# Kernel tuning notes

Measured on AMD Instinct MI355X. Metric: run time of the kernel, lower is better.

The kernel has to match this reference:

```python
import jax, jax.numpy as jnp
import numpy as np


def setup_inputs() -> dict:
    key = jax.random.key(0)
    ks = jax.random.split(key, 5)
    B, T, I, H = 32, 2048, 512, 512
    scale = 1.0 / np.sqrt(H)
    return {
        "x": jax.random.normal(ks[0], (B, T, I), dtype=jnp.float32),
        "h_0": jnp.zeros((B, H), dtype=jnp.float32),
        "Wx": jax.random.normal(ks[1], (H, I), dtype=jnp.float32) * scale,
        "bx": jax.random.normal(ks[2], (H,), dtype=jnp.float32) * scale,
        "Wh": jax.random.normal(ks[3], (H, H), dtype=jnp.float32) * scale,
        "bh": jax.random.normal(ks[4], (H,), dtype=jnp.float32) * scale,
    }


def reference(x, h_0, Wx, bx, Wh, bh):
    # Precompute input projection for all timesteps in one big GEMM: [B,T,H]
    x_proj = jnp.einsum("bti,hi->bth", x, Wx) + bx + bh

    def step(h, xp_t):  # h: [B,H], xp_t: [B,H]
        h_new = jnp.tanh(xp_t + h @ Wh.T)
        return h_new, h_new

    # scan over time axis: move T to leading dim
    h_last, outs = jax.lax.scan(step, h_0, jnp.swapaxes(x_proj, 0, 1))
    outputs = jnp.swapaxes(outs, 0, 1)  # [B,T,H]
    return outputs, h_last
```

## Files before the change

kernel.cpp:

```cpp
#include <hip/hip_runtime.h>


constexpr int Bb = 32, Tt = 2048, Ii = 512, Hh = 512;
constexpr int NP = 8;
constexpr int RP = Hh / NP;

static __device__ __forceinline__ float fast_tanh(float x) {
    float ax = fabsf(x);
    float e = __expf(-2.0f * ax);
    float r = (1.0f - e) / (1.0f + e);
    return copysignf(r, x);
}

__global__ __launch_bounds__(256, 2)
void xproj_gemm(const float* __restrict__ x, const float* __restrict__ Wx,
                const float* __restrict__ bx, const float* __restrict__ bh,
                float* __restrict__ xp)
{
    constexpr int BM = 128, BK = 16, LDT = BM + 4;
    __shared__ float As[BK][LDT];
    __shared__ float Bs[BK][LDT];

    const int tid = threadIdx.x;
    const int m0 = blockIdx.x * BM;
    const int n0 = blockIdx.y * BM;
    const int lrow = tid >> 1;
    const int lkh  = (tid & 1) * 8;
    const int tx = tid & 15, ty = tid >> 4;

    float acc[2][2][4][4] = {};

    for (int k0 = 0; k0 < Ii; k0 += BK) {
        float4 a0 = *reinterpret_cast<const float4*>(&x[(size_t)(m0 + lrow) * Ii + k0 + lkh]);
        float4 a1 = *reinterpret_cast<const float4*>(&x[(size_t)(m0 + lrow) * Ii + k0 + lkh + 4]);
        float4 b0 = *reinterpret_cast<const float4*>(&Wx[(size_t)(n0 + lrow) * Ii + k0 + lkh]);
        float4 b1 = *reinterpret_cast<const float4*>(&Wx[(size_t)(n0 + lrow) * Ii + k0 + lkh + 4]);
        __syncthreads();
        As[lkh + 0][lrow] = a0.x; As[lkh + 1][lrow] = a0.y;
        As[lkh + 2][lrow] = a0.z; As[lkh + 3][lrow] = a0.w;
        As[lkh + 4][lrow] = a1.x; As[lkh + 5][lrow] = a1.y;
        As[lkh + 6][lrow] = a1.z; As[lkh + 7][lrow] = a1.w;
        Bs[lkh + 0][lrow] = b0.x; Bs[lkh + 1][lrow] = b0.y;
        Bs[lkh + 2][lrow] = b0.z; Bs[lkh + 3][lrow] = b0.w;
        Bs[lkh + 4][lrow] = b1.x; Bs[lkh + 5][lrow] = b1.y;
        Bs[lkh + 6][lrow] = b1.z; Bs[lkh + 7][lrow] = b1.w;
        __syncthreads();
        #pragma unroll
        for (int k = 0; k < BK; ++k) {
            float4 av[2], bv[2];
            av[0] = *reinterpret_cast<const float4*>(&As[k][ty * 4]);
            av[1] = *reinterpret_cast<const float4*>(&As[k][64 + ty * 4]);
            bv[0] = *reinterpret_cast<const float4*>(&Bs[k][tx * 4]);
            bv[1] = *reinterpret_cast<const float4*>(&Bs[k][64 + tx * 4]);
            #pragma unroll
            for (int rh = 0; rh < 2; ++rh) {
                const float* ap = reinterpret_cast<const float*>(&av[rh]);
                #pragma unroll
                for (int ch = 0; ch < 2; ++ch) {
                    const float* bp = reinterpret_cast<const float*>(&bv[ch]);
                    #pragma unroll
                    for (int i = 0; i < 4; ++i)
                        #pragma unroll
                        for (int j = 0; j < 4; ++j)
                            acc[rh][ch][i][j] += ap[i] * bp[j];
                }
            }
        }
    }

    float4 bias[2];
    #pragma unroll
    for (int ch = 0; ch < 2; ++ch) {
        int cb = n0 + ch * 64 + tx * 4;
        bias[ch] = make_float4(bx[cb] + bh[cb], bx[cb + 1] + bh[cb + 1],
                               bx[cb + 2] + bh[cb + 2], bx[cb + 3] + bh[cb + 3]);
    }
    #pragma unroll
    for (int rh = 0; rh < 2; ++rh)
        #pragma unroll
        for (int i = 0; i < 4; ++i) {
            size_t row = (size_t)(m0 + rh * 64 + ty * 4 + i);
            #pragma unroll
            for (int ch = 0; ch < 2; ++ch) {
                const float* bp = reinterpret_cast<const float*>(&bias[ch]);
                float4 v = make_float4(acc[rh][ch][i][0] + bp[0], acc[rh][ch][i][1] + bp[1],
                                       acc[rh][ch][i][2] + bp[2], acc[rh][ch][i][3] + bp[3]);
                *reinterpret_cast<float4*>(&xp[row * Hh + n0 + ch * 64 + tx * 4]) = v;
            }
        }
}

__global__ void zero_xbuf(unsigned long long* __restrict__ xb)
{
    xb[(size_t)blockIdx.x * 512 + threadIdx.x] = 0ull;
}

__global__ __launch_bounds__(512, 1)
void rnn_scan_mb(const float* __restrict__ Wh, const float* __restrict__ h0,
                 float* __restrict__ out, unsigned long long* __restrict__ xbuf)
{
    const int bid = blockIdx.x;
    const int c = bid & 31;
    const int P = bid >> 5;
    const int tid = threadIdx.x;
    const int w = tid >> 6;
    const int lane = tid & 63;

    __shared__ float hscratch[NP][68];
    __shared__ float pacc[2][NP][68];

    float4 wreg[16];
    #pragma unroll
    for (int k = 0; k < 16; ++k) {
        const float* ap = &Wh[(size_t)(P * RP + lane) * Hh + w * 64 + 4 * k];
        asm volatile("global_load_dwordx4 %0, %1, off"
                     : "=v"(wreg[k]) : "v"(ap));
    }
    asm volatile("s_waitcnt vmcnt(0)" ::: "memory");

    float* ob = out + (size_t)c * Tt * Hh;
    unsigned long long* xb = xbuf + (size_t)c * 2 * Hh;

    float hcur = h0[(size_t)c * Hh + w * 64 + lane];
    float xp_cur = (w == P) ? ob[P * RP + lane] : 0.f;

    for (int t = 0; t < Tt; ++t) {
        const int d = t & 1;

        hscratch[w][lane] = hcur;
        asm volatile("s_waitcnt lgkmcnt(0)" ::: "memory");

        float a0 = 0.f, a1 = 0.f, a2 = 0.f, a3 = 0.f;
        #pragma unroll
        for (int k = 0; k < 16; k += 4) {
            float4 h0v = *reinterpret_cast<const float4*>(&hscratch[w][4 * k]);
            float4 h1v = *reinterpret_cast<const float4*>(&hscratch[w][4 * k + 4]);
            float4 h2v = *reinterpret_cast<const float4*>(&hscratch[w][4 * k + 8]);
            float4 h3v = *reinterpret_cast<const float4*>(&hscratch[w][4 * k + 12]);
            const float* w0 = reinterpret_cast<const float*>(&wreg[k]);
            const float* w1 = reinterpret_cast<const float*>(&wreg[k + 1]);
            const float* w2 = reinterpret_cast<const float*>(&wreg[k + 2]);
            const float* w3 = reinterpret_cast<const float*>(&wreg[k + 3]);
            a0 += w0[0] * h0v.x; a0 += w0[1] * h0v.y; a0 += w0[2] * h0v.z; a0 += w0[3] * h0v.w;
            a1 += w1[0] * h1v.x; a1 += w1[1] * h1v.y; a1 += w1[2] * h1v.z; a1 += w1[3] * h1v.w;
            a2 += w2[0] * h2v.x; a2 += w2[1] * h2v.y; a2 += w2[2] * h2v.z; a2 += w2[3] * h2v.w;
            a3 += w3[0] * h3v.x; a3 += w3[1] * h3v.y; a3 += w3[2] * h3v.z; a3 += w3[3] * h3v.w;
        }
        pacc[d][w][lane] = (a0 + a1) + (a2 + a3);
        __syncthreads();

        if (w == P) {
            float s = xp_cur;
            #pragma unroll
            for (int g = 0; g < NP; ++g) s += pacc[d][g][lane];
            float hval = fast_tanh(s);
            hcur = hval;
            if (t + 1 < Tt) {
                unsigned long long msg =
                    ((unsigned long long)(unsigned)(t + 1) << 32) |
                    (unsigned long long)__float_as_uint(hval);
                __hip_atomic_store(&xb[(size_t)d * Hh + P * RP + lane], msg,
                                   __ATOMIC_RELAXED, __HIP_MEMORY_SCOPE_AGENT);
                ob[(size_t)t * Hh + P * RP + lane] = hval;
                xp_cur = ob[(size_t)(t + 1) * Hh + P * RP + lane];
            } else {
                ob[(size_t)t * Hh + P * RP + lane] = hval;
                out[(size_t)Bb * Tt * Hh + (size_t)c * Hh + P * RP + lane] = hval;
            }
        } else if (t + 1 < Tt) {
            const unsigned want = (unsigned)(t + 1);
            unsigned long long msg;
            do {
                msg = __hip_atomic_load(&xb[(size_t)d * Hh + w * RP + lane],
                                        __ATOMIC_RELAXED, __HIP_MEMORY_SCOPE_AGENT);
            } while ((unsigned)(msg >> 32) != want);
            hcur = __uint_as_float((unsigned)msg);
        }
    }
}

__global__ __launch_bounds__(512)
void rnn_scan_sb(const float* __restrict__ W, const float* __restrict__ h0,
                 float* __restrict__ out)
{
    const int b = blockIdx.x;
    const int j = threadIdx.x;
    __shared__ float hsb[2][Hh];
    hsb[0][j] = h0[(size_t)b * Hh + j];
    __syncthreads();

    float* ob = out + (size_t)b * Tt * Hh;
    const float* wbase = W + (size_t)j * Hh;

    float xp_cur = ob[j];
    int cur = 0;
    for (int t = 0; t < Tt; ++t) {
        float xp_next = (t + 1 < Tt) ? ob[(size_t)(t + 1) * Hh + j] : 0.0f;
        float4 a = make_float4(xp_cur, 0.0f, 0.0f, 0.0f);
        const float* h = hsb[cur];
        #pragma unroll 8
        for (int c4 = 0; c4 < Hh / 4; ++c4) {
            float4 wv = *reinterpret_cast<const float4*>(&wbase[c4 * 4]);
            float4 hv = *reinterpret_cast<const float4*>(&h[c4 * 4]);
            a.x += wv.x * hv.x; a.y += wv.y * hv.y;
            a.z += wv.z * hv.z; a.w += wv.w * hv.w;
        }
        float hn = tanhf((a.x + a.y) + (a.z + a.w));
        hsb[cur ^ 1][j] = hn;
        ob[(size_t)t * Hh + j] = hn;
        xp_cur = xp_next;
        cur ^= 1;
        __syncthreads();
    }
    out[(size_t)Bb * Tt * Hh + (size_t)b * Hh + j] = hsb[cur][j];
}

extern "C" void kernel_launch(void* const* d_in, const int* in_sizes, int n_in,
                              void* d_out, int out_size, void* d_ws, size_t ws_size,
                              hipStream_t stream)
{
    const float* x  = (const float*)d_in[0];
    const float* h0 = (const float*)d_in[1];
    const float* Wx = (const float*)d_in[2];
    const float* bx = (const float*)d_in[3];
    const float* Wh = (const float*)d_in[4];
    const float* bh = (const float*)d_in[5];
    float* out = (float*)d_out;

    dim3 g1(Bb * Tt / 128, Hh / 128);
    xproj_gemm<<<g1, 256, 0, stream>>>(x, Wx, bx, bh, out);

    const size_t xb_bytes = (size_t)Bb * 2 * Hh * sizeof(unsigned long long);
    if (ws_size >= xb_bytes) {
        unsigned long long* xbuf = (unsigned long long*)d_ws;
        zero_xbuf<<<64, 512, 0, stream>>>(xbuf);
        void* args[] = {(void*)&Wh, (void*)&h0, (void*)&out, (void*)&xbuf};
        hipLaunchCooperativeKernel((void*)rnn_scan_mb, dim3(NP * Bb), dim3(512),
                                   args, 0, stream);
    } else {
        rnn_scan_sb<<<Bb, Hh, 0, stream>>>(Wh, h0, out);
    }
}
```

Baseline: 3.298 ms.

## Add XCD-local L2 fast path for cross-block hidden-state exchange

Each block reads its XCC id from a hardware register and publishes it. After a grid sync, each batch group checks whether all eight of its blocks sit on the same XCD. Producers now write every message twice: a plain store to an L2-local buffer and an agent-scope atomic store to a second buffer. When a group is co-located, consumers first poll the L2-local copy with sc0 loads, up to a fixed number of tries, and fall back to the device-coherent buffer otherwise. The aim is to cut the latency of the per-timestep exchange, at the cost of a duplicated store per step, a grid sync at startup, and a gain that depends on where blocks are placed.

```diff
diff --git a/kernel.cpp b/kernel.cpp
--- a/kernel.cpp
+++ b/kernel.cpp
@@ -1,4 +1,5 @@
 #include <hip/hip_runtime.h>
+#include <hip/hip_cooperative_groups.h>
 
 
 constexpr int Bb = 32, Tt = 2048, Ii = 512, Hh = 512;
@@ -97,7 +98,9 @@
 
 __global__ __launch_bounds__(512, 1)
 void rnn_scan_mb(const float* __restrict__ Wh, const float* __restrict__ h0,
-                 float* __restrict__ out, unsigned long long* __restrict__ xbuf)
+                 float* __restrict__ out, unsigned long long* __restrict__ xbL2,
+                 unsigned long long* __restrict__ xbIC,
+                 unsigned int* __restrict__ xcc_arr)
 {
     const int bid = blockIdx.x;
     const int c = bid & 31;
@@ -108,6 +111,13 @@
 
     __shared__ float hscratch[NP][68];
     __shared__ float pacc[2][NP][68];
+    __shared__ unsigned int same_sh;
+
+    unsigned int myxcc;
+    asm volatile("s_getreg_b32 %0, hwreg(20, 0, 32)" : "=s"(myxcc));
+    if (tid == 0)
+        __hip_atomic_store(&xcc_arr[bid], myxcc, __ATOMIC_RELAXED,
+                           __HIP_MEMORY_SCOPE_AGENT);
 
     float4 wreg[16];
     #pragma unroll
@@ -119,10 +129,22 @@
     asm volatile("s_waitcnt vmcnt(0)" ::: "memory");
 
     float* ob = out + (size_t)c * Tt * Hh;
-    unsigned long long* xb = xbuf + (size_t)c * 2 * Hh;
+    unsigned long long* xL = xbL2 + (size_t)c * 2 * Hh;
+    unsigned long long* xI = xbIC + (size_t)c * 2 * Hh;
 
     float hcur = h0[(size_t)c * Hh + w * 64 + lane];
     float xp_cur = (w == P) ? ob[P * RP + lane] : 0.f;
+
+    cooperative_groups::this_grid().sync();
+    if (tid == 0) {
+        unsigned int s = 1;
+        for (int p = 0; p < NP; ++p)
+            s &= (__hip_atomic_load(&xcc_arr[(p << 5) | c], __ATOMIC_RELAXED,
+                                    __HIP_MEMORY_SCOPE_AGENT) == myxcc) ? 1u : 0u;
+        same_sh = s;
+    }
+    __syncthreads();
+    const bool samexcd = (same_sh != 0);
 
     for (int t = 0; t < Tt; ++t) {
         const int d = t & 1;
@@ -159,7 +181,10 @@
                 unsigned long long msg =
                     ((unsigned long long)(unsigned)(t + 1) << 32) |
                     (unsigned long long)__float_as_uint(hval);
-                __hip_atomic_store(&xb[(size_t)d * Hh + P * RP + lane], msg,
+                unsigned long long* paL = &xL[(size_t)d * Hh + P * RP + lane];
+                asm volatile("global_store_dwordx2 %0, %1, off"
+                             :: "v"(paL), "v"(msg) : "memory");
+                __hip_atomic_store(&xI[(size_t)d * Hh + P * RP + lane], msg,
                                    __ATOMIC_RELAXED, __HIP_MEMORY_SCOPE_AGENT);
                 ob[(size_t)t * Hh + P * RP + lane] = hval;
                 xp_cur = ob[(size_t)(t + 1) * Hh + P * RP + lane];
@@ -169,12 +194,29 @@
             }
         } else if (t + 1 < Tt) {
             const unsigned want = (unsigned)(t + 1);
-            unsigned long long msg;
-            do {
-                msg = __hip_atomic_load(&xb[(size_t)d * Hh + w * RP + lane],
-                                        __ATOMIC_RELAXED, __HIP_MEMORY_SCOPE_AGENT);
-            } while ((unsigned)(msg >> 32) != want);
-            hcur = __uint_as_float((unsigned)msg);
+            bool got = false;
+            unsigned val = 0;
+            if (samexcd) {
+                const unsigned long long* paL = &xL[(size_t)d * Hh + w * RP + lane];
+                uint2 m;
+                #pragma unroll 1
+                for (int it = 0; it < 12; ++it) {
+                    asm volatile("global_load_dwordx2 %0, %1, off sc0\n\t"
+                                 "s_waitcnt vmcnt(0)"
+                                 : "=v"(m) : "v"(paL) : "memory");
+                    if (m.y == want) { val = m.x; got = true; break; }
+                }
+            }
+            if (!got) {
+                const unsigned long long* paI = &xI[(size_t)d * Hh + w * RP + lane];
+                unsigned long long msg;
+                do {
+                    msg = __hip_atomic_load(paI, __ATOMIC_RELAXED,
+                                            __HIP_MEMORY_SCOPE_AGENT);
+                } while ((unsigned)(msg >> 32) != want);
+                val = (unsigned)msg;
+            }
+            hcur = __uint_as_float(val);
         }
     }
 }
@@ -230,11 +272,15 @@
     dim3 g1(Bb * Tt / 128, Hh / 128);
     xproj_gemm<<<g1, 256, 0, stream>>>(x, Wx, bx, bh, out);
 
-    const size_t xb_bytes = (size_t)Bb * 2 * Hh * sizeof(unsigned long long);
-    if (ws_size >= xb_bytes) {
-        unsigned long long* xbuf = (unsigned long long*)d_ws;
-        zero_xbuf<<<64, 512, 0, stream>>>(xbuf);
-        void* args[] = {(void*)&Wh, (void*)&h0, (void*)&out, (void*)&xbuf};
+    const size_t xb_bytes  = (size_t)Bb * 2 * Hh * sizeof(unsigned long long);
+    const size_t xcc_bytes = 256 * sizeof(unsigned int);
+    if (ws_size >= 2 * xb_bytes + xcc_bytes) {
+        unsigned long long* xbL2 = (unsigned long long*)d_ws;
+        unsigned long long* xbIC = (unsigned long long*)((char*)d_ws + xb_bytes);
+        unsigned int* xcc_arr = (unsigned int*)((char*)d_ws + 2 * xb_bytes);
+        zero_xbuf<<<128, 512, 0, stream>>>((unsigned long long*)d_ws);
+        void* args[] = {(void*)&Wh, (void*)&h0, (void*)&out,
+                        (void*)&xbL2, (void*)&xbIC, (void*)&xcc_arr};
         hipLaunchCooperativeKernel((void*)rnn_scan_mb, dim3(NP * Bb), dim3(512),
                                    args, 0, stream);
     } else {
```

Result: slower. 5.410 ms (+64.1%).

## Switch recurrent scan to column-split partitioning with all-to-all partial-sum exchange

Applied to the files above, without the earlier changes.

Each block now holds a column slice of Wh for all 512 output rows instead of a row slice, so it computes partial dot products for every hidden unit from only its own slice of h. Partials are exchanged through tagged 64-bit messages in a larger workspace, and every warp reduces its own slice and applies tanh locally. The removed cost is the serialized step where one warp reduced, activated and then broadcast h before others could proceed. The next-step input projection is also prefetched earlier. In exchange each step sends 8x more global messages and each block polls on seven peers, which risks more atomic and memory traffic.

```diff
diff --git a/kernel.cpp b/kernel.cpp
--- a/kernel.cpp
+++ b/kernel.cpp
@@ -97,7 +97,7 @@
 
 __global__ __launch_bounds__(512, 1)
 void rnn_scan_mb(const float* __restrict__ Wh, const float* __restrict__ h0,
-                 float* __restrict__ out, unsigned long long* __restrict__ xbuf)
+                 float* __restrict__ out, unsigned long long* __restrict__ xpart)
 {
     const int bid = blockIdx.x;
     const int c = bid & 31;
@@ -106,37 +106,41 @@
     const int w = tid >> 6;
     const int lane = tid & 63;
 
-    __shared__ float hscratch[NP][68];
-    __shared__ float pacc[2][NP][68];
+    __shared__ float hpriv[NP][68];
+    __shared__ float red[2][NP][68];
 
     float4 wreg[16];
     #pragma unroll
     for (int k = 0; k < 16; ++k) {
-        const float* ap = &Wh[(size_t)(P * RP + lane) * Hh + w * 64 + 4 * k];
+        const float* ap = &Wh[(size_t)tid * Hh + P * RP + 4 * k];
         asm volatile("global_load_dwordx4 %0, %1, off"
                      : "=v"(wreg[k]) : "v"(ap));
     }
     asm volatile("s_waitcnt vmcnt(0)" ::: "memory");
 
     float* ob = out + (size_t)c * Tt * Hh;
-    unsigned long long* xb = xbuf + (size_t)c * 2 * Hh;
-
-    float hcur = h0[(size_t)c * Hh + w * 64 + lane];
-    float xp_cur = (w == P) ? ob[P * RP + lane] : 0.f;
+    unsigned long long* xbc = xpart + (size_t)c * 2 * NP * Hh / NP * NP;
+    xbc = xpart + (size_t)c * (2 * NP * 512 / 1);
+
+    hpriv[w][lane] = h0[(size_t)c * Hh + P * RP + lane];
+
+    float xp_cur = ob[P * RP + lane];
+    __syncthreads();
 
     for (int t = 0; t < Tt; ++t) {
         const int d = t & 1;
 
-        hscratch[w][lane] = hcur;
-        asm volatile("s_waitcnt lgkmcnt(0)" ::: "memory");
-
+        float xp_nxt = 0.f;
+        if (t + 1 < Tt) xp_nxt = ob[(size_t)(t + 1) * Hh + P * RP + lane];
+
+        const float* hp = hpriv[w];
         float a0 = 0.f, a1 = 0.f, a2 = 0.f, a3 = 0.f;
         #pragma unroll
         for (int k = 0; k < 16; k += 4) {
-            float4 h0v = *reinterpret_cast<const float4*>(&hscratch[w][4 * k]);
-            float4 h1v = *reinterpret_cast<const float4*>(&hscratch[w][4 * k + 4]);
-            float4 h2v = *reinterpret_cast<const float4*>(&hscratch[w][4 * k + 8]);
-            float4 h3v = *reinterpret_cast<const float4*>(&hscratch[w][4 * k + 12]);
+            float4 h0v = *reinterpret_cast<const float4*>(&hp[4 * k]);
+            float4 h1v = *reinterpret_cast<const float4*>(&hp[4 * k + 4]);
+            float4 h2v = *reinterpret_cast<const float4*>(&hp[4 * k + 8]);
+            float4 h3v = *reinterpret_cast<const float4*>(&hp[4 * k + 12]);
             const float* w0 = reinterpret_cast<const float*>(&wreg[k]);
             const float* w1 = reinterpret_cast<const float*>(&wreg[k + 1]);
             const float* w2 = reinterpret_cast<const float*>(&wreg[k + 2]);
@@ -146,36 +150,41 @@
             a2 += w2[0] * h2v.x; a2 += w2[1] * h2v.y; a2 += w2[2] * h2v.z; a2 += w2[3] * h2v.w;
             a3 += w3[0] * h3v.x; a3 += w3[1] * h3v.y; a3 += w3[2] * h3v.z; a3 += w3[3] * h3v.w;
         }
-        pacc[d][w][lane] = (a0 + a1) + (a2 + a3);
-        __syncthreads();
-
+        float partial = (a0 + a1) + (a2 + a3);
+
+        unsigned long long* xb = xpart + ((size_t)c * 2 + d) * (NP * 512);
         if (w == P) {
-            float s = xp_cur;
-            #pragma unroll
-            for (int g = 0; g < NP; ++g) s += pacc[d][g][lane];
-            float hval = fast_tanh(s);
-            hcur = hval;
-            if (t + 1 < Tt) {
-                unsigned long long msg =
-                    ((unsigned long long)(unsigned)(t + 1) << 32) |
-                    (unsigned long long)__float_as_uint(hval);
-                __hip_atomic_store(&xb[(size_t)d * Hh + P * RP + lane], msg,
-                                   __ATOMIC_RELAXED, __HIP_MEMORY_SCOPE_AGENT);
-                ob[(size_t)t * Hh + P * RP + lane] = hval;
-                xp_cur = ob[(size_t)(t + 1) * Hh + P * RP + lane];
-            } else {
-                ob[(size_t)t * Hh + P * RP + lane] = hval;
+            red[d][P][lane] = partial;
+        } else {
+            unsigned long long msg =
+                ((unsigned long long)(unsigned)(t + 1) << 32) |
+                (unsigned long long)__float_as_uint(partial);
+            __hip_atomic_store(&xb[(size_t)P * 512 + tid], msg,
+                               __ATOMIC_RELAXED, __HIP_MEMORY_SCOPE_AGENT);
+            const unsigned want = (unsigned)(t + 1);
+            const unsigned long long* pa = &xb[(size_t)w * 512 + P * RP + lane];
+            unsigned long long msg2;
+            do {
+                msg2 = __hip_atomic_load(pa, __ATOMIC_RELAXED,
+                                         __HIP_MEMORY_SCOPE_AGENT);
+            } while ((unsigned)(msg2 >> 32) != want);
+            red[d][w][lane] = __uint_as_float((unsigned)msg2);
+        }
+        __syncthreads();
+
+        float s = xp_cur;
+        #pragma unroll
+        for (int g = 0; g < NP; ++g) s += red[d][g][lane];
+        float hval = fast_tanh(s);
+        hpriv[w][lane] = hval;
+        asm volatile("s_waitcnt lgkmcnt(0)" ::: "memory");
+
+        if (w == P) {
+            ob[(size_t)t * Hh + P * RP + lane] = hval;
+            if (t + 1 >= Tt)
                 out[(size_t)Bb * Tt * Hh + (size_t)c * Hh + P * RP + lane] = hval;
-            }
-        } else if (t + 1 < Tt) {
-            const unsigned want = (unsigned)(t + 1);
-            unsigned long long msg;
-            do {
-                msg = __hip_atomic_load(&xb[(size_t)d * Hh + w * RP + lane],
-                                        __ATOMIC_RELAXED, __HIP_MEMORY_SCOPE_AGENT);
-            } while ((unsigned)(msg >> 32) != want);
-            hcur = __uint_as_float((unsigned)msg);
-        }
+        }
+        xp_cur = xp_nxt;
     }
 }
 
@@ -230,11 +239,11 @@
     dim3 g1(Bb * Tt / 128, Hh / 128);
     xproj_gemm<<<g1, 256, 0, stream>>>(x, Wx, bx, bh, out);
 
-    const size_t xb_bytes = (size_t)Bb * 2 * Hh * sizeof(unsigned long long);
+    const size_t xb_bytes = (size_t)Bb * 2 * NP * 512 * sizeof(unsigned long long);
     if (ws_size >= xb_bytes) {
-        unsigned long long* xbuf = (unsigned long long*)d_ws;
-        zero_xbuf<<<64, 512, 0, stream>>>(xbuf);
-        void* args[] = {(void*)&Wh, (void*)&h0, (void*)&out, (void*)&xbuf};
+        unsigned long long* xpart = (unsigned long long*)d_ws;
+        zero_xbuf<<<512, 512, 0, stream>>>(xpart);
+        void* args[] = {(void*)&Wh, (void*)&h0, (void*)&out, (void*)&xpart};
         hipLaunchCooperativeKernel((void*)rnn_scan_mb, dim3(NP * Bb), dim3(512),
                                    args, 0, stream);
     } else {
```

Measured after the change: 3.377 ms. +2.4%, slower.
